# Performance work log

Hardware: AMD Instinct MI355X
Metric: run time of the kernel (lower is better)

Reference implementation:

```python
import jax, jax.numpy as jnp
import numpy as np

# candidate init bones from the original module
INIT_BONES = np.array([0, 1, 2, 4, 5, 6, 11, 12, 13, 16, 17, 18, 19, 20], dtype=np.int32)
SOFTMAX_TEMP = 20.0
DIST_THRESH = 0.1
NEG_INF = -1e4


def setup_inputs() -> dict:
    key = jax.random.key(0)
    k1, k2, k3 = jax.random.split(key, 3)
    B, N, J = 1, 65536, 25
    D, H, W = 32, 128, 128  # d = res // z_ratio, h = w = res
    x = jax.random.uniform(k1, (B, N, 3), jnp.float32, -0.9, 0.9)
    # bone transforms ~ identity + noise, valid homogeneous last row
    tfs = jnp.eye(4, dtype=jnp.float32)[None, None] + 0.05 * jax.random.normal(k2, (B, J, 4, 4), jnp.float32)
    tfs = tfs.at[:, :, 3, :].set(jnp.array([0.0, 0.0, 0.0, 1.0], jnp.float32))
    lbs_voxel = 0.1 * jax.random.normal(k3, (1, J, D, H, W), jnp.float32)
    init_bones = jnp.asarray(INIT_BONES)
    return {"x": x, "tfs": tfs, "lbs_voxel": lbs_voxel, "init_bones": init_bones}


def trilinear_sample(vox, coords):
    """vox: [J,D,H,W]; coords: [...,3] in [-1,1], x->W, y->H, z->D.
    align_corners=True, border padding. Returns [..., J]."""
    J, D, H, W = vox.shape
    cx = jnp.clip((coords[..., 0] + 1.0) * 0.5 * (W - 1), 0.0, W - 1)
    cy = jnp.clip((coords[..., 1] + 1.0) * 0.5 * (H - 1), 0.0, H - 1)
    cz = jnp.clip((coords[..., 2] + 1.0) * 0.5 * (D - 1), 0.0, D - 1)
    x0 = jnp.floor(cx).astype(jnp.int32); x1 = jnp.minimum(x0 + 1, W - 1)
    y0 = jnp.floor(cy).astype(jnp.int32); y1 = jnp.minimum(y0 + 1, H - 1)
    z0 = jnp.floor(cz).astype(jnp.int32); z1 = jnp.minimum(z0 + 1, D - 1)
    fx = cx - x0; fy = cy - y0; fz = cz - z0
    vf = vox.reshape(J, -1)

    def gather(zi, yi, xi):
        idx = (zi * H + yi) * W + xi
        return jnp.moveaxis(jnp.take(vf, idx, axis=1), 0, -1)  # [..., J]

    fx = fx[..., None]; fy = fy[..., None]; fz = fz[..., None]
    c00 = gather(z0, y0, x0) * (1 - fx) + gather(z0, y0, x1) * fx
    c01 = gather(z0, y1, x0) * (1 - fx) + gather(z0, y1, x1) * fx
    c10 = gather(z1, y0, x0) * (1 - fx) + gather(z1, y0, x1) * fx
    c11 = gather(z1, y1, x0) * (1 - fx) + gather(z1, y1, x1) * fx
    c0 = c00 * (1 - fy) + c01 * fy
    c1 = c10 * (1 - fy) + c11 * fy
    return c0 * (1 - fz) + c1 * fz


def reference(x, tfs, lbs_voxel, init_bones):
    """Voxel skinning query + multi-init candidate warp + argmax aggregation (agg).
    x: [B,N,3] deformed points; tfs: [B,J,4,4]; lbs_voxel: [1,J,D,H,W]; init_bones: [I]."""
    B, N, _ = x.shape
    xh = jnp.concatenate([x, jnp.ones_like(x[..., :1])], axis=-1)  # [B,N,4]
    # multi-init candidates: invert each init bone transform
    Ti = tfs[:, init_bones]                       # [B,I,4,4]
    Tinv = jnp.linalg.inv(Ti)
    xc = jnp.einsum('bipq,bnq->bnip', Tinv, xh)[..., :3]  # [B,N,I,3] canonical candidates
    # skinning weights: trilinear voxel query + tempered softmax over bones
    w = trilinear_sample(lbs_voxel[0], xc)        # [B,N,I,J]
    w = jax.nn.softmax(SOFTMAX_TEMP * w, axis=-1)
    # fused forward LBS: x_warp = sum_j w_j * (T_j @ x_cano)
    xc_h = jnp.concatenate([xc, jnp.ones_like(xc[..., :1])], axis=-1)  # [B,N,I,4]
    Txc = jnp.einsum('bjpq,bniq->bnijp', tfs[:, :, :3, :], xc_h)        # [B,N,I,J,3]
    x_warp = jnp.einsum('bnij,bnijp->bnip', w, Txc)                     # [B,N,I,3]
    # root-finding residual -> density per candidate, invalid candidates masked out
    err = jnp.linalg.norm(x_warp - x[:, :, None, :], axis=-1)  # [B,N,I]
    mask = err < DIST_THRESH
    density = jnp.where(mask, -err, NEG_INF)[..., None]        # [B,N,I,1]
    features = w[..., :15]                                     # [B,N,I,15]
    # agg(): argmax over candidate dim I, gather features/warp/mask at winner
    idx = jnp.argmax(density[..., 0], axis=-1)                 # [B,N]
    d_agg = jnp.max(density, axis=-2)                          # [B,N,1]
    f_agg = jnp.take_along_axis(features, idx[..., None, None], axis=-2)[..., 0, :]  # [B,N,15]
    w_agg = jnp.take_along_axis(xc, idx[..., None, None], axis=-2)[..., 0, :]        # [B,N,3]
    m_agg = jnp.take_along_axis(mask, idx[..., None], axis=-1)[..., 0]               # [B,N]
    return d_agg, f_agg, m_agg, w_agg
```

## Files before the change

kernel.cpp:

```cpp
#include <hip/hip_runtime.h>
#include <math.h>

#define NJ 25
#define NJP 32
#define VD 32
#define VH 128
#define VW 128
#define TEMP 20.0f
#define NEGINF (-10000.0f)
#define DHW (VD*VH*VW)
#define NCELL 4096
#define TINV_FLOATS 256


__global__ void invert_tfs_kernel(const float* __restrict__ tfs,
                                  const int* __restrict__ bones,
                                  float* __restrict__ tinv, int ni) {
    int t = threadIdx.x;
    if (t >= ni) return;
    const float* T = tfs + (size_t)bones[t] * 16;
    double r00=T[0], r01=T[1], r02=T[2],  tx=T[3];
    double r10=T[4], r11=T[5], r12=T[6],  ty=T[7];
    double r20=T[8], r21=T[9], r22=T[10], tz=T[11];
    double c00 = r11*r22 - r12*r21;
    double c01 = r12*r20 - r10*r22;
    double c02 = r10*r21 - r11*r20;
    double det = r00*c00 + r01*c01 + r02*c02;
    double id  = 1.0/det;
    double i00 = c00*id;
    double i01 = (r02*r21 - r01*r22)*id;
    double i02 = (r01*r12 - r02*r11)*id;
    double i10 = c01*id;
    double i11 = (r00*r22 - r02*r20)*id;
    double i12 = (r02*r10 - r00*r12)*id;
    double i20 = c02*id;
    double i21 = (r01*r20 - r00*r21)*id;
    double i22 = (r00*r11 - r01*r10)*id;
    double itx = -(i00*tx + i01*ty + i02*tz);
    double ity = -(i10*tx + i11*ty + i12*tz);
    double itz = -(i20*tx + i21*ty + i22*tz);
    float* o = tinv + t*12;
    o[0]=(float)i00; o[1]=(float)i01; o[2] =(float)i02; o[3] =(float)itx;
    o[4]=(float)i10; o[5]=(float)i11; o[6] =(float)i12; o[7] =(float)ity;
    o[8]=(float)i20; o[9]=(float)i21; o[10]=(float)i22; o[11]=(float)itz;
}

__global__ __launch_bounds__(256) void transpose_vox_kernel(const float* __restrict__ vox,
                                                            float* __restrict__ vt) {
    __shared__ float lds[NJ*129];
    int row = blockIdx.x;
    int t = threadIdx.x;
    for (int idx = t; idx < NJ*VW; idx += 256) {
        int j  = idx >> 7;
        int xx = idx & 127;
        lds[j*129 + xx] = vox[(size_t)j*DHW + (size_t)row*VW + xx];
    }
    __syncthreads();
    float* out = vt + (size_t)row * (VW*NJP);
    for (int idx = t; idx < VW*NJP; idx += 256) {
        int xx = idx >> 5;
        int j  = idx & 31;
        out[idx] = (j < NJ) ? lds[j*129 + xx] : 0.0f;
    }
}

__device__ __forceinline__ int cell_of(float v) {
    int c = (int)((v + 1.0f) * 8.0f);
    return min(max(c, 0), 15);
}
__device__ __forceinline__ int morton12(int ix, int iy, int iz) {
    int m = 0;
    #pragma unroll
    for (int b = 0; b < 4; ++b)
        m |= (((ix>>b)&1)<<(3*b)) | (((iy>>b)&1)<<(3*b+1)) | (((iz>>b)&1)<<(3*b+2));
    return m;
}
__global__ void zero_hist_kernel(int* hist) {
    int g = blockIdx.x*256 + threadIdx.x;
    if (g < NCELL) hist[g] = 0;
}
__global__ void hist_kernel(const float* __restrict__ x, int* __restrict__ hist, int N) {
    int g = blockIdx.x*256 + threadIdx.x;
    if (g >= N) return;
    int m = morton12(cell_of(x[g*3+0]), cell_of(x[g*3+1]), cell_of(x[g*3+2]));
    atomicAdd(&hist[m], 1);
}
__global__ __launch_bounds__(1024) void scan_kernel(const int* __restrict__ hist,
                                                    int* __restrict__ offs) {
    __shared__ int part[1024];
    int t = threadIdx.x;
    int4 h = ((const int4*)hist)[t];
    int s = h.x + h.y + h.z + h.w;
    part[t] = s;
    __syncthreads();
    for (int off = 1; off < 1024; off <<= 1) {
        int v = (t >= off) ? part[t-off] : 0;
        __syncthreads();
        part[t] += v;
        __syncthreads();
    }
    int excl = part[t] - s;
    offs[4*t+0] = excl;
    offs[4*t+1] = excl + h.x;
    offs[4*t+2] = excl + h.x + h.y;
    offs[4*t+3] = excl + h.x + h.y + h.z;
}
__global__ void scatter_kernel(const float* __restrict__ x, int* __restrict__ offs,
                               int* __restrict__ perm, int N) {
    int g = blockIdx.x*256 + threadIdx.x;
    if (g >= N) return;
    int m = morton12(cell_of(x[g*3+0]), cell_of(x[g*3+1]), cell_of(x[g*3+2]));
    int pos = atomicAdd(&offs[m], 1);
    perm[pos] = g;
}

__device__ __forceinline__ float f4g(const float4 v, int k) {
    return k==0 ? v.x : k==1 ? v.y : k==2 ? v.z : v.w;
}

#define CH_BODY(jj, vv) do {                                              \
    float ev = __expf(TEMP * (vv));                                       \
    s_sum += ev;                                                          \
    const float* M_ = &tfs[(jj)*16];                                      \
    E0 += ev*M_[0]; E1  += ev*M_[1];  E2  += ev*M_[2];  E3  += ev*M_[3];  \
    E4 += ev*M_[4]; E5  += ev*M_[5];  E6  += ev*M_[6];  E7  += ev*M_[7];  \
    E8 += ev*M_[8]; E9  += ev*M_[9];  E10 += ev*M_[10]; E11 += ev*M_[11]; \
    if ((jj) < 15) myE[curOff + (jj)] = ev;                               \
} while (0)

template<bool VT>
__global__ __launch_bounds__(256) void deformer_kernel(
        const float* __restrict__ x,
        const float* __restrict__ tfs,
        const float* __restrict__ vsrc,
        const float* __restrict__ tinv,
        const int* __restrict__ perm,
        float* __restrict__ out, int N, int ni) {
    __shared__ float s_feat[256*33];
    int t   = threadIdx.x;

    int nwg = gridDim.x;
    int q = nwg >> 3, r = nwg & 7;
    int xcd = blockIdx.x & 7, blk = blockIdx.x >> 3;
    int lb = (xcd < r ? xcd*(q+1) : r*(q+1) + (xcd-r)*q) + blk;

    int ns  = lb*128 + (t >> 1);
    int sub = t & 1;
    if (ns >= N) return;
    int n = perm ? perm[ns] : ns;

    float px = x[n*3+0], py = x[n*3+1], pz = x[n*3+2];
    float* myE = &s_feat[t*33];

    float bestD = -3.0e38f;
    int   bestIdx = 0x7fffffff;
    int   curOff = 0, bestOff = 0;
    float bInvs = 1.0f;
    float bcx = 0.f, bcy = 0.f, bcz = 0.f;

    #pragma unroll 1
    for (int i = sub; i < ni; i += 2) {
        const float* Ti = &tinv[i*12];
        float cx = Ti[0]*px + Ti[1]*py + Ti[2] *pz + Ti[3];
        float cy = Ti[4]*px + Ti[5]*py + Ti[6] *pz + Ti[7];
        float cz = Ti[8]*px + Ti[9]*py + Ti[10]*pz + Ti[11];

        float gx = fminf(fmaxf((cx + 1.0f) * (0.5f*(VW-1)), 0.0f), (float)(VW-1));
        float gy = fminf(fmaxf((cy + 1.0f) * (0.5f*(VH-1)), 0.0f), (float)(VH-1));
        float gz = fminf(fmaxf((cz + 1.0f) * (0.5f*(VD-1)), 0.0f), (float)(VD-1));
        int x0 = (int)gx, y0 = (int)gy, z0 = (int)gz;
        int x1 = min(x0+1, VW-1), y1 = min(y0+1, VH-1), z1 = min(z0+1, VD-1);
        float fx = gx - (float)x0, fy = gy - (float)y0, fz = gz - (float)z0;
        float ax = 1.0f - fx, ay = 1.0f - fy, az = 1.0f - fz;
        float w000 = ax*ay*az, w001 = fx*ay*az, w010 = ax*fy*az, w011 = fx*fy*az;
        float w100 = ax*ay*fz, w101 = fx*ay*fz, w110 = ax*fy*fz, w111 = fx*fy*fz;

        float s_sum = 0.0f;
        float E0=0,E1=0,E2=0,E3=0,E4=0,E5=0,E6=0,E7=0,E8=0,E9=0,E10=0,E11=0;

        if (VT) {
            int o000 = ((z0*VH + y0)*VW + x0) * NJP;
            int dz = (z1 - z0) * (VH*VW*NJP);
            int dy = (y1 - y0) * (VW*NJP);
            int dx = (x1 - x0) * NJP;
            int o001 = o000 + dx,      o010 = o000 + dy,      o011 = o000 + dy + dx;
            int o100 = o000 + dz,      o101 = o000 + dz + dx;
            int o110 = o000 + dz + dy, o111 = o000 + dz + dy + dx;

            #pragma unroll
            for (int j4 = 0; j4 < 7; ++j4) {
                const int jb = j4*4;
                float4 a000 = *(const float4*)&vsrc[o000 + jb];
                float4 a001 = *(const float4*)&vsrc[o001 + jb];
                float4 a010 = *(const float4*)&vsrc[o010 + jb];
                float4 a011 = *(const float4*)&vsrc[o011 + jb];
                float4 a100 = *(const float4*)&vsrc[o100 + jb];
                float4 a101 = *(const float4*)&vsrc[o101 + jb];
                float4 a110 = *(const float4*)&vsrc[o110 + jb];
                float4 a111 = *(const float4*)&vsrc[o111 + jb];
                #pragma unroll
                for (int k = 0; k < 4; ++k) {
                    const int j = jb + k;
                    if (j < NJ) {
                        float v = f4g(a000,k)*w000 + f4g(a001,k)*w001
                                + f4g(a010,k)*w010 + f4g(a011,k)*w011
                                + f4g(a100,k)*w100 + f4g(a101,k)*w101
                                + f4g(a110,k)*w110 + f4g(a111,k)*w111;
                        CH_BODY(j, v);
                    }
                }
            }
        } else {
            int b000 = (z0*VH + y0)*VW + x0;
            int dz = (z1 - z0) * (VH*VW);
            int dy = (y1 - y0) * VW;
            int dx = (x1 - x0);
            #pragma unroll
            for (int j = 0; j < NJ; ++j) {
                const float* vj = vsrc + (size_t)j*DHW + b000;
                float v = vj[0]*w000        + vj[dx]*w001
                        + vj[dy]*w010       + vj[dy+dx]*w011
                        + vj[dz]*w100       + vj[dz+dx]*w101
                        + vj[dz+dy]*w110    + vj[dz+dy+dx]*w111;
                CH_BODY(j, v);
            }
        }

        float invs = 1.0f / s_sum;
        float wxp = (E0*cx + E1*cy + E2 *cz + E3 ) * invs;
        float wyp = (E4*cx + E5*cy + E6 *cz + E7 ) * invs;
        float wzp = (E8*cx + E9*cy + E10*cz + E11) * invs;
        float dxp = wxp - px, dyp = wyp - py, dzp = wzp - pz;
        float err = sqrtf(dxp*dxp + dyp*dyp + dzp*dzp);
        float d = (err < 0.1f) ? -err : NEGINF;

        if (d > bestD || (d == bestD && i < bestIdx)) {
            bestD = d; bestIdx = i;
            bestOff = curOff; curOff ^= 16;
            bInvs = invs;
            bcx = cx; bcy = cy; bcz = cz;
        }
    }

    float od = __shfl_xor(bestD, 1); int oi = __shfl_xor(bestIdx, 1);
    if (od > bestD || (od == bestD && oi < bestIdx)) { bestD = od; bestIdx = oi; }

    if (sub == (bestIdx & 1)) {
        float* o_d = out;
        float* o_f = out + N;
        float* o_m = out + (size_t)N*16;
        float* o_w = out + (size_t)N*17;
        o_d[n] = bestD;
        #pragma unroll
        for (int k = 0; k < 15; ++k) o_f[(size_t)n*15 + k] = myE[bestOff + k] * bInvs;
        o_m[n] = (bestD > -9999.0f) ? 1.0f : 0.0f;
        o_w[n*3+0] = bcx; o_w[n*3+1] = bcy; o_w[n*3+2] = bcz;
    }
}

extern "C" void kernel_launch(void* const* d_in, const int* in_sizes, int n_in,
                              void* d_out, int out_size, void* d_ws, size_t ws_size,
                              hipStream_t stream) {
    const float* x     = (const float*)d_in[0];
    const float* tfs   = (const float*)d_in[1];
    const float* vox   = (const float*)d_in[2];
    const int*   bones = (const int*)  d_in[3];
    int N  = in_sizes[0] / 3;
    int ni = in_sizes[3];

    float* ws = (float*)d_ws;
    size_t vt_off    = (size_t)TINV_FLOATS + NCELL*2 + (size_t)N;
    size_t vt_floats = (size_t)DHW * NJP;
    size_t need_all  = vt_off + vt_floats;

    float* tinv = ws;
    int*   hist = (int*)(ws + TINV_FLOATS);
    int*   offs = hist + NCELL;
    int*   perm = offs + NCELL;
    float* vt   = ws + vt_off;

    bool useVT = ws_size >= need_all * sizeof(float);
    int nblk = (N + 127) / 128;

    hipLaunchKernelGGL(invert_tfs_kernel, dim3(1), dim3(64), 0, stream,
                       tfs, bones, tinv, ni);
    if (useVT) {
        hipLaunchKernelGGL(transpose_vox_kernel, dim3(VD*VH), dim3(256), 0, stream,
                           vox, vt);
        hipLaunchKernelGGL(zero_hist_kernel, dim3((NCELL+255)/256), dim3(256), 0, stream, hist);
        hipLaunchKernelGGL(hist_kernel, dim3((N+255)/256), dim3(256), 0, stream, x, hist, N);
        hipLaunchKernelGGL(scan_kernel, dim3(1), dim3(1024), 0, stream, hist, offs);
        hipLaunchKernelGGL(scatter_kernel, dim3((N+255)/256), dim3(256), 0, stream, x, offs, perm, N);
        hipLaunchKernelGGL((deformer_kernel<true>), dim3(nblk), dim3(256), 0, stream,
                           x, tfs, vt, tinv, perm, (float*)d_out, N, ni);
    } else {
        hipLaunchKernelGGL((deformer_kernel<false>), dim3(nblk), dim3(256), 0, stream,
                           x, tfs, vox, tinv, (const int*)nullptr,
                           (float*)d_out, N, ni);
    }
}
```

Before: 257.6 us.

## Split candidates across four lanes, fuse setup kernels, vectorize voxel transpose

Each point is now handled by four lanes instead of two, with a second shuffle reduction, so there are twice as many blocks and less serial candidate work per thread. The 12 per-candidate matrix accumulators are replaced by three warped-position accumulators, which lowers register pressure at the cost of more FMAs per bone. The winning candidate's inverse sum is stored in LDS, and its canonical point is recomputed at the end instead of being kept in registers. The transform-inversion and histogram-zeroing kernels are merged into one launch, and the voxel transpose now uses float4 loads and stores.

```diff
diff --git a/kernel.cpp b/kernel.cpp
--- a/kernel.cpp
+++ b/kernel.cpp
@@ -13,36 +13,42 @@
 #define TINV_FLOATS 256
 
 
-__global__ void invert_tfs_kernel(const float* __restrict__ tfs,
-                                  const int* __restrict__ bones,
-                                  float* __restrict__ tinv, int ni) {
-    int t = threadIdx.x;
-    if (t >= ni) return;
-    const float* T = tfs + (size_t)bones[t] * 16;
-    double r00=T[0], r01=T[1], r02=T[2],  tx=T[3];
-    double r10=T[4], r11=T[5], r12=T[6],  ty=T[7];
-    double r20=T[8], r21=T[9], r22=T[10], tz=T[11];
-    double c00 = r11*r22 - r12*r21;
-    double c01 = r12*r20 - r10*r22;
-    double c02 = r10*r21 - r11*r20;
-    double det = r00*c00 + r01*c01 + r02*c02;
-    double id  = 1.0/det;
-    double i00 = c00*id;
-    double i01 = (r02*r21 - r01*r22)*id;
-    double i02 = (r01*r12 - r02*r11)*id;
-    double i10 = c01*id;
-    double i11 = (r00*r22 - r02*r20)*id;
-    double i12 = (r02*r10 - r00*r12)*id;
-    double i20 = c02*id;
-    double i21 = (r01*r20 - r00*r21)*id;
-    double i22 = (r00*r11 - r01*r10)*id;
-    double itx = -(i00*tx + i01*ty + i02*tz);
-    double ity = -(i10*tx + i11*ty + i12*tz);
-    double itz = -(i20*tx + i21*ty + i22*tz);
-    float* o = tinv + t*12;
-    o[0]=(float)i00; o[1]=(float)i01; o[2] =(float)i02; o[3] =(float)itx;
-    o[4]=(float)i10; o[5]=(float)i11; o[6] =(float)i12; o[7] =(float)ity;
-    o[8]=(float)i20; o[9]=(float)i21; o[10]=(float)i22; o[11]=(float)itz;
+__global__ void setup_kernel(const float* __restrict__ tfs,
+                             const int* __restrict__ bones,
+                             float* __restrict__ tinv,
+                             int* __restrict__ hist, int ni) {
+    int b = blockIdx.x, t = threadIdx.x;
+    if (b == 0) {
+        if (t >= ni) return;
+        const float* T = tfs + (size_t)bones[t] * 16;
+        double r00=T[0], r01=T[1], r02=T[2],  tx=T[3];
+        double r10=T[4], r11=T[5], r12=T[6],  ty=T[7];
+        double r20=T[8], r21=T[9], r22=T[10], tz=T[11];
+        double c00 = r11*r22 - r12*r21;
+        double c01 = r12*r20 - r10*r22;
+        double c02 = r10*r21 - r11*r20;
+        double det = r00*c00 + r01*c01 + r02*c02;
+        double id  = 1.0/det;
+        double i00 = c00*id;
+        double i01 = (r02*r21 - r01*r22)*id;
+        double i02 = (r01*r12 - r02*r11)*id;
+        double i10 = c01*id;
+        double i11 = (r00*r22 - r02*r20)*id;
+        double i12 = (r02*r10 - r00*r12)*id;
+        double i20 = c02*id;
+        double i21 = (r01*r20 - r00*r21)*id;
+        double i22 = (r00*r11 - r01*r10)*id;
+        double itx = -(i00*tx + i01*ty + i02*tz);
+        double ity = -(i10*tx + i11*ty + i12*tz);
+        double itz = -(i20*tx + i21*ty + i22*tz);
+        float* o = tinv + t*12;
+        o[0]=(float)i00; o[1]=(float)i01; o[2] =(float)i02; o[3] =(float)itx;
+        o[4]=(float)i10; o[5]=(float)i11; o[6] =(float)i12; o[7] =(float)ity;
+        o[8]=(float)i20; o[9]=(float)i21; o[10]=(float)i22; o[11]=(float)itz;
+    } else {
+        int g = (b-1)*256 + t;
+        if (g < NCELL) hist[g] = 0;
+    }
 }
 
 __global__ __launch_bounds__(256) void transpose_vox_kernel(const float* __restrict__ vox,
@@ -50,17 +56,25 @@
     __shared__ float lds[NJ*129];
     int row = blockIdx.x;
     int t = threadIdx.x;
-    for (int idx = t; idx < NJ*VW; idx += 256) {
-        int j  = idx >> 7;
-        int xx = idx & 127;
-        lds[j*129 + xx] = vox[(size_t)j*DHW + (size_t)row*VW + xx];
+    const float4* v4 = (const float4*)vox;
+    for (int idx = t; idx < NJ*32; idx += 256) {
+        int j  = idx >> 5;
+        int x4 = idx & 31;
+        float4 v = v4[(size_t)j*(DHW/4) + (size_t)row*32 + x4];
+        float* l = &lds[j*129 + x4*4];
+        l[0]=v.x; l[1]=v.y; l[2]=v.z; l[3]=v.w;
     }
     __syncthreads();
-    float* out = vt + (size_t)row * (VW*NJP);
-    for (int idx = t; idx < VW*NJP; idx += 256) {
-        int xx = idx >> 5;
-        int j  = idx & 31;
-        out[idx] = (j < NJ) ? lds[j*129 + xx] : 0.0f;
+    float4* out4 = (float4*)(vt + (size_t)row * (VW*NJP));
+    for (int idx = t; idx < (VW*NJP)/4; idx += 256) {
+        int xx = idx >> 3;
+        int jq = (idx & 7) * 4;
+        float4 o;
+        o.x = (jq+0 < NJ) ? lds[(jq+0)*129 + xx] : 0.0f;
+        o.y = (jq+1 < NJ) ? lds[(jq+1)*129 + xx] : 0.0f;
+        o.z = (jq+2 < NJ) ? lds[(jq+2)*129 + xx] : 0.0f;
+        o.w = (jq+3 < NJ) ? lds[(jq+3)*129 + xx] : 0.0f;
+        out4[idx] = o;
     }
 }
 
@@ -74,10 +88,6 @@
     for (int b = 0; b < 4; ++b)
         m |= (((ix>>b)&1)<<(3*b)) | (((iy>>b)&1)<<(3*b+1)) | (((iz>>b)&1)<<(3*b+2));
     return m;
-}
-__global__ void zero_hist_kernel(int* hist) {
-    int g = blockIdx.x*256 + threadIdx.x;
-    if (g < NCELL) hist[g] = 0;
 }
 __global__ void hist_kernel(const float* __restrict__ x, int* __restrict__ hist, int N) {
     int g = blockIdx.x*256 + threadIdx.x;
@@ -122,9 +132,9 @@
     float ev = __expf(TEMP * (vv));                                       \
     s_sum += ev;                                                          \
     const float* M_ = &tfs[(jj)*16];                                      \
-    E0 += ev*M_[0]; E1  += ev*M_[1];  E2  += ev*M_[2];  E3  += ev*M_[3];  \
-    E4 += ev*M_[4]; E5  += ev*M_[5];  E6  += ev*M_[6];  E7  += ev*M_[7];  \
-    E8 += ev*M_[8]; E9  += ev*M_[9];  E10 += ev*M_[10]; E11 += ev*M_[11]; \
+    wx += ev*(M_[0]*cx + M_[1]*cy + M_[2] *cz + M_[3]);                   \
+    wy += ev*(M_[4]*cx + M_[5]*cy + M_[6] *cz + M_[7]);                   \
+    wz += ev*(M_[8]*cx + M_[9]*cy + M_[10]*cz + M_[11]);                  \
     if ((jj) < 15) myE[curOff + (jj)] = ev;                               \
 } while (0)
 
@@ -144,8 +154,8 @@
     int xcd = blockIdx.x & 7, blk = blockIdx.x >> 3;
     int lb = (xcd < r ? xcd*(q+1) : r*(q+1) + (xcd-r)*q) + blk;
 
-    int ns  = lb*128 + (t >> 1);
-    int sub = t & 1;
+    int ns  = lb*64 + (t >> 2);
+    int sub = t & 3;
     if (ns >= N) return;
     int n = perm ? perm[ns] : ns;
 
@@ -155,11 +165,9 @@
     float bestD = -3.0e38f;
     int   bestIdx = 0x7fffffff;
     int   curOff = 0, bestOff = 0;
-    float bInvs = 1.0f;
-    float bcx = 0.f, bcy = 0.f, bcz = 0.f;
 
     #pragma unroll 1
-    for (int i = sub; i < ni; i += 2) {
+    for (int i = sub; i < ni; i += 4) {
         const float* Ti = &tinv[i*12];
         float cx = Ti[0]*px + Ti[1]*py + Ti[2] *pz + Ti[3];
         float cy = Ti[4]*px + Ti[5]*py + Ti[6] *pz + Ti[7];
@@ -176,7 +184,7 @@
         float w100 = ax*ay*fz, w101 = fx*ay*fz, w110 = ax*fy*fz, w111 = fx*fy*fz;
 
         float s_sum = 0.0f;
-        float E0=0,E1=0,E2=0,E3=0,E4=0,E5=0,E6=0,E7=0,E8=0,E9=0,E10=0,E11=0;
+        float wx = 0.0f, wy = 0.0f, wz = 0.0f;
 
         if (VT) {
             int o000 = ((z0*VH + y0)*VW + x0) * NJP;
@@ -227,34 +235,37 @@
         }
 
         float invs = 1.0f / s_sum;
-        float wxp = (E0*cx + E1*cy + E2 *cz + E3 ) * invs;
-        float wyp = (E4*cx + E5*cy + E6 *cz + E7 ) * invs;
-        float wzp = (E8*cx + E9*cy + E10*cz + E11) * invs;
-        float dxp = wxp - px, dyp = wyp - py, dzp = wzp - pz;
+        float dxp = wx*invs - px, dyp = wy*invs - py, dzp = wz*invs - pz;
         float err = sqrtf(dxp*dxp + dyp*dyp + dzp*dzp);
         float d = (err < 0.1f) ? -err : NEGINF;
 
         if (d > bestD || (d == bestD && i < bestIdx)) {
             bestD = d; bestIdx = i;
+            myE[curOff + 15] = invs;
             bestOff = curOff; curOff ^= 16;
-            bInvs = invs;
-            bcx = cx; bcy = cy; bcz = cz;
         }
     }
 
     float od = __shfl_xor(bestD, 1); int oi = __shfl_xor(bestIdx, 1);
     if (od > bestD || (od == bestD && oi < bestIdx)) { bestD = od; bestIdx = oi; }
-
-    if (sub == (bestIdx & 1)) {
+    od = __shfl_xor(bestD, 2); oi = __shfl_xor(bestIdx, 2);
+    if (od > bestD || (od == bestD && oi < bestIdx)) { bestD = od; bestIdx = oi; }
+
+    if (sub == (bestIdx & 3)) {
+        const float* Ti = &tinv[bestIdx*12];
+        float cx = Ti[0]*px + Ti[1]*py + Ti[2] *pz + Ti[3];
+        float cy = Ti[4]*px + Ti[5]*py + Ti[6] *pz + Ti[7];
+        float cz = Ti[8]*px + Ti[9]*py + Ti[10]*pz + Ti[11];
+        float invs = myE[bestOff + 15];
         float* o_d = out;
         float* o_f = out + N;
         float* o_m = out + (size_t)N*16;
         float* o_w = out + (size_t)N*17;
         o_d[n] = bestD;
         #pragma unroll
-        for (int k = 0; k < 15; ++k) o_f[(size_t)n*15 + k] = myE[bestOff + k] * bInvs;
+        for (int k = 0; k < 15; ++k) o_f[(size_t)n*15 + k] = myE[bestOff + k] * invs;
         o_m[n] = (bestD > -9999.0f) ? 1.0f : 0.0f;
-        o_w[n*3+0] = bcx; o_w[n*3+1] = bcy; o_w[n*3+2] = bcz;
+        o_w[n*3+0] = cx; o_w[n*3+1] = cy; o_w[n*3+2] = cz;
     }
 }
 
@@ -280,14 +291,13 @@
     float* vt   = ws + vt_off;
 
     bool useVT = ws_size >= need_all * sizeof(float);
-    int nblk = (N + 127) / 128;
-
-    hipLaunchKernelGGL(invert_tfs_kernel, dim3(1), dim3(64), 0, stream,
-                       tfs, bones, tinv, ni);
+    int nblk = (N + 63) / 64;
+
+    hipLaunchKernelGGL(setup_kernel, dim3(1 + NCELL/256), dim3(256), 0, stream,
+                       tfs, bones, tinv, hist, ni);
     if (useVT) {
         hipLaunchKernelGGL(transpose_vox_kernel, dim3(VD*VH), dim3(256), 0, stream,
                            vox, vt);
-        hipLaunchKernelGGL(zero_hist_kernel, dim3((NCELL+255)/256), dim3(256), 0, stream, hist);
         hipLaunchKernelGGL(hist_kernel, dim3((N+255)/256), dim3(256), 0, stream, x, hist, N);
         hipLaunchKernelGGL(scan_kernel, dim3(1), dim3(1024), 0, stream, hist, offs);
         hipLaunchKernelGGL(scatter_kernel, dim3((N+255)/256), dim3(256), 0, stream, x, offs, perm, N);
```

Result: slower. 273.0 us (+6.0%).
